# Kernel tuning notes

Measured on AMD Instinct MI355X. Metric: run time of the kernel, lower is better.

The kernel has to match this reference:

```python
import jax, jax.numpy as jnp
import numpy as np

EMBED_DIM = 64
NUM_ITEM = 1000000
BATCH = 131072
SEQ_LEN = 5
# fixed_arc = "AND,0,~1;OR,2,3;AND,5,6;OR,~7,4" parsed: (module, (pos, negated), (pos, negated))
ARC = [("AND", (0, False), (1, True)),
       ("OR",  (2, False), (3, False)),
       ("AND", (5, False), (6, False)),
       ("OR",  (7, True),  (4, False))]


def setup_inputs() -> dict:
    key = jax.random.key(0)
    ks = jax.random.split(key, 20)
    std = 0.01  # init_params: normal(0, 0.01)
    inp = {}
    inp["seq"] = jax.random.randint(ks[0], (BATCH, SEQ_LEN), 0, NUM_ITEM, dtype=jnp.int32)
    inp["pos_target"] = jax.random.randint(ks[1], (BATCH,), 0, NUM_ITEM, dtype=jnp.int32)
    inp["neg_target"] = jax.random.randint(ks[2], (BATCH,), 0, NUM_ITEM, dtype=jnp.int32)
    inp["item_embed"] = std * jax.random.normal(ks[3], (NUM_ITEM, EMBED_DIM), dtype=jnp.float32)
    t = jax.random.uniform(ks[4], (EMBED_DIM,), minval=0.0, maxval=0.1, dtype=jnp.float32)
    inp["true_vec"] = t / jnp.maximum(jnp.linalg.norm(t), 1e-12)
    inp["not_W1"] = std * jax.random.normal(ks[5], (EMBED_DIM, EMBED_DIM), dtype=jnp.float32)
    inp["not_b1"] = std * jax.random.normal(ks[6], (EMBED_DIM,), dtype=jnp.float32)
    inp["not_W2"] = std * jax.random.normal(ks[7], (EMBED_DIM, EMBED_DIM), dtype=jnp.float32)
    inp["not_b2"] = std * jax.random.normal(ks[8], (EMBED_DIM,), dtype=jnp.float32)
    inp["and_W1"] = std * jax.random.normal(ks[9], (2 * EMBED_DIM, EMBED_DIM), dtype=jnp.float32)
    inp["and_b1"] = std * jax.random.normal(ks[10], (EMBED_DIM,), dtype=jnp.float32)
    inp["and_W2"] = std * jax.random.normal(ks[11], (EMBED_DIM, EMBED_DIM), dtype=jnp.float32)
    inp["and_b2"] = std * jax.random.normal(ks[12], (EMBED_DIM,), dtype=jnp.float32)
    inp["or_W1"] = std * jax.random.normal(ks[13], (2 * EMBED_DIM, EMBED_DIM), dtype=jnp.float32)
    inp["or_b1"] = std * jax.random.normal(ks[14], (EMBED_DIM,), dtype=jnp.float32)
    inp["or_W2"] = std * jax.random.normal(ks[15], (EMBED_DIM, EMBED_DIM), dtype=jnp.float32)
    inp["or_b2"] = std * jax.random.normal(ks[16], (EMBED_DIM,), dtype=jnp.float32)
    return inp


def _mlp(x, W1, b1, W2, b2):
    # _get_ln_module(num_layers=2, dropout=0): Linear -> LeakyReLU -> Dropout(0) -> Linear
    h = jax.nn.leaky_relu(x @ W1 + b1, negative_slope=0.01)
    return h @ W2 + b2


def reference(seq, pos_target, neg_target, item_embed, true_vec,
              not_W1, not_b1, not_W2, not_b2,
              and_W1, and_b1, and_W2, and_b2,
              or_W1, or_b1, or_W2, or_b2):
    NOT = lambda x: _mlp(x, not_W1, not_b1, not_W2, not_b2)
    AND = lambda x: _mlp(x, and_W1, and_b1, and_W2, and_b2)
    OR = lambda x: _mlp(x, or_W1, or_b1, or_W2, or_b2)
    mods = {"AND": AND, "OR": OR}

    intermediates = {}

    def get_input(pos, neg):
        if pos < SEQ_LEN:
            e = item_embed[seq[:, pos]]  # [B, D] embedding gather
        else:
            e = intermediates[pos]
        return NOT(e) if neg else e

    out = None
    for layer_id, (name, (p1, n1), (p2, n2)) in enumerate(ARC):
        i1 = get_input(p1, n1)
        i2 = get_input(p2, n2)
        out = mods[name](jnp.concatenate((i1, i2), axis=-1))
        intermediates[SEQ_LEN + layer_id] = out

    enc_not = NOT(out)  # [B, D]
    pos_e = item_embed[pos_target]
    neg_e = item_embed[neg_target]
    encoded_pos = OR(jnp.concatenate((enc_not, pos_e), axis=-1))
    encoded_neg = OR(jnp.concatenate((enc_not, neg_e), axis=-1))
    encoded = jnp.concatenate((encoded_pos, encoded_neg), axis=0)  # [2B, D]

    # cosine similarity vs 'true' anchor, amplified by 10 (cos_amplify_factor)
    eps = 1e-8
    num = encoded @ true_vec
    denom = jnp.maximum(jnp.linalg.norm(encoded, axis=-1), eps) * jnp.maximum(jnp.linalg.norm(true_vec), eps)
    prediction = (num / denom) * 10.0
    return prediction
```

## Files before the change

### kernel.cpp

```cpp
#include <hip/hip_runtime.h>
#include <stdint.h>
#include <math.h>

#define BATCH 131072

typedef __attribute__((ext_vector_type(8)))  short short8;
typedef __attribute__((ext_vector_type(16))) float float16;

#define WS_LO_OFF 65536
#define WS_TN_OFF 131072

__global__ __launch_bounds__(256)
void prep_kernel(const float* __restrict__ tvec,
                 const float* __restrict__ nW1, const float* __restrict__ nW2,
                 const float* __restrict__ aW1, const float* __restrict__ aW2,
                 const float* __restrict__ oW1, const float* __restrict__ oW2,
                 char* __restrict__ ws)
{
    const int id = blockIdx.x * 256 + threadIdx.x;
    if (id == 0) {
        float s = 0.f;
        for (int j = 0; j < 64; ++j) s = fmaf(tvec[j], tvec[j], s);
        *(float*)(ws + WS_TN_OFF) = fmaxf(sqrtf(s), 1e-8f);
    }
    const float* srcs[8] = { nW1, nW2, aW1, aW1 + 4096, aW2, oW1, oW1 + 4096, oW2 };
    const int u    = id >> 12;
    const int e    = id & 4095;
    const int j    = e & 7;
    const int lane = (e >> 3) & 63;
    const int f    = e >> 9;
    const int nt   = f & 1, kc = f >> 1;
    const int k    = kc * 16 + (lane >> 5) * 8 + j;
    const int n    = nt * 32 + (lane & 31);
    const float v  = srcs[u][k * 64 + n];
    const uint32_t b  = __float_as_uint(v);
    const uint32_t hb = b & 0xffff0000u;
    const uint32_t lo = __float_as_uint(v - __uint_as_float(hb));
    ((uint16_t*)(ws + u * 8192 + f * 1024 + lane * 16))[j]             = (uint16_t)(b  >> 16);
    ((uint16_t*)(ws + WS_LO_OFF + u * 8192 + f * 1024 + lane * 16))[j] = (uint16_t)(lo >> 16);
}

union S8 { short8 s; uint32_t u[4]; };
union F8 { float f[8]; uint32_t u[8]; float4 v4[2]; };

struct Frag { short8 hi[4]; short8 lo[4]; };

__global__ __launch_bounds__(256)
void logicnet_mfma(const int* __restrict__ seq, const int* __restrict__ post,
                   const int* __restrict__ negt, const float* __restrict__ E,
                   const float* __restrict__ tvec,
                   const float* __restrict__ nb1, const float* __restrict__ nb2,
                   const float* __restrict__ ab1, const float* __restrict__ ab2,
                   const float* __restrict__ ob1, const float* __restrict__ ob2,
                   const char* __restrict__ ws, float* __restrict__ out)
{
    __shared__ uint32_t lds[4 * 2112];
    const int tid  = threadIdx.x;
    const int wid  = tid >> 6;
    const int lane = tid & 63;
    const int m    = lane & 31;
    const int h    = lane >> 5;
    const int tile = blockIdx.x * 4 + wid;
    const int rowbase = tile * 32;
    uint32_t* const stage = &lds[wid * 2112];

    const float tn = *(const float*)(ws + WS_TN_OFF);

    float nb1v[2] = { nb1[m], nb1[32 + m] };
    float nb2v[2] = { nb2[m], nb2[32 + m] };
    float ab1v[2] = { ab1[m], ab1[32 + m] };
    float ab2v[2] = { ab2[m], ab2[32 + m] };
    float ob1v[2] = { ob1[m], ob1[32 + m] };
    float ob2v[2] = { ob2[m], ob2[32 + m] };

    const int rr = rowbase + m;
    const int s0 = seq[rr * 5 + 0], s1i = seq[rr * 5 + 1], s2 = seq[rr * 5 + 2];
    const int s3 = seq[rr * 5 + 3], s4 = seq[rr * 5 + 4];
    const int ip = post[rr], im = negt[rr];

    float16 acc[2], accE[2];

    auto initacc = [&](const float* bv) {
#pragma unroll
        for (int nt = 0; nt < 2; ++nt)
#pragma unroll
            for (int i = 0; i < 16; ++i) acc[nt][i] = bv[nt];
    };

    auto ua = [&](const Frag& x, int u) {
        const char* base = ws + u * 8192 + lane * 16;
#pragma unroll
        for (int kc = 0; kc < 4; ++kc) {
#pragma unroll
            for (int nt = 0; nt < 2; ++nt) {
                const int off = (kc * 2 + nt) * 1024;
                short8 whi = *(const short8*)(base + off);
                short8 wlo = *(const short8*)(base + WS_LO_OFF + off);
                acc[nt] = __builtin_amdgcn_mfma_f32_32x32x16_bf16(x.hi[kc], whi, acc[nt], 0, 0, 0);
                acc[nt] = __builtin_amdgcn_mfma_f32_32x32x16_bf16(x.lo[kc], whi, acc[nt], 0, 0, 0);
                acc[nt] = __builtin_amdgcn_mfma_f32_32x32x16_bf16(x.hi[kc], wlo, acc[nt], 0, 0, 0);
            }
        }
    };

    auto epi_store = [&](bool lrelu) {
#pragma unroll
        for (int nt = 0; nt < 2; ++nt) {
            const int c = nt * 32 + m;
#pragma unroll
            for (int g = 0; g < 4; ++g)
#pragma unroll
                for (int q = 0; q < 4; ++q) {
                    const int r = q + 8 * g + 4 * h;
                    float v = acc[nt][g * 4 + q];
                    if (lrelu) v = fmaxf(v, 0.01f * v);
                    const uint32_t uu = __float_as_uint(v);
                    const uint32_t hb = uu & 0xffff0000u;
                    const uint32_t lo = __float_as_uint(v - __uint_as_float(hb));
                    stage[r * 66 + c] = hb | (lo >> 16);
                }
        }
    };

    auto load_frags = [&](Frag& x) {
#pragma unroll
        for (int kc = 0; kc < 4; ++kc) {
            const uint32_t* p = &stage[m * 66 + kc * 16 + h * 8];
            uint32_t w[8];
#pragma unroll
            for (int i = 0; i < 8; ++i) w[i] = p[i];
            S8 hi, lo;
#pragma unroll
            for (int i = 0; i < 4; ++i) {
                hi.u[i] = (w[2 * i] >> 16)      | (w[2 * i + 1] & 0xffff0000u);
                lo.u[i] = (w[2 * i] & 0xffffu)  | (w[2 * i + 1] << 16);
            }
            x.hi[kc] = hi.s; x.lo[kc] = lo.s;
        }
    };

    auto gather = [&](int idx, Frag& x) {
        const float4* e = (const float4*)(E + (size_t)idx * 64 + h * 8);
#pragma unroll
        for (int kc = 0; kc < 4; ++kc) {
            F8 xf8;
            xf8.v4[0] = e[kc * 4];
            xf8.v4[1] = e[kc * 4 + 1];
            uint32_t lu[8];
#pragma unroll
            for (int i = 0; i < 8; ++i) {
                const float hf = __uint_as_float(xf8.u[i] & 0xffff0000u);
                lu[i] = __float_as_uint(xf8.f[i] - hf);
            }
            S8 hi, lo;
#pragma unroll
            for (int i = 0; i < 4; ++i) {
                hi.u[i] = (xf8.u[2 * i] >> 16) | (xf8.u[2 * i + 1] & 0xffff0000u);
                lo.u[i] = (lu[2 * i] >> 16)    | (lu[2 * i + 1] & 0xffff0000u);
            }
            x.hi[kc] = hi.s; x.lo[kc] = lo.s;
        }
    };

    auto epi_reduce = [&](float* outp) {
#pragma unroll
        for (int nt = 0; nt < 2; ++nt) {
            const int c = nt * 32 + m;
#pragma unroll
            for (int g = 0; g < 4; ++g)
#pragma unroll
                for (int q = 0; q < 4; ++q) {
                    const int r = q + 8 * g + 4 * h;
                    stage[r * 66 + c] = __float_as_uint(acc[nt][g * 4 + q]);
                }
        }
        float num = 0.f, ss = 0.f;
        const float* tp = tvec + h * 32;
        const uint32_t* xp = &stage[m * 66 + h * 32];
#pragma unroll
        for (int i = 0; i < 32; i += 2) {
            const float x0 = __uint_as_float(xp[i]);
            const float x1 = __uint_as_float(xp[i + 1]);
            num = fmaf(x0, tp[i], fmaf(x1, tp[i + 1], num));
            ss  = fmaf(x0, x0, fmaf(x1, x1, ss));
        }
        num += __shfl_xor(num, 32, 64);
        ss  += __shfl_xor(ss, 32, 64);
        if (h == 0) outp[m] = num / (fmaxf(sqrtf(ss), 1e-8f) * tn) * 10.0f;
    };

    Frag xf, i6f;

    gather(s2, xf); initacc(ob1v); ua(xf, 5);
    gather(s3, xf); ua(xf, 6);
    epi_store(true);  load_frags(xf);
    initacc(ob2v); ua(xf, 7);
    epi_store(false); load_frags(i6f);

    gather(s1i, xf); initacc(nb1v); ua(xf, 0);
    epi_store(true);  load_frags(xf);
    initacc(nb2v); ua(xf, 1);
    epi_store(false); load_frags(xf);

    initacc(ab1v); ua(xf, 3);
    gather(s0, xf); ua(xf, 2);
    epi_store(true);  load_frags(xf);
    initacc(ab2v); ua(xf, 4);
    epi_store(false); load_frags(xf);

    initacc(ab1v); ua(xf, 2); ua(i6f, 3);
    epi_store(true);  load_frags(xf);
    initacc(ab2v); ua(xf, 4);
    epi_store(false); load_frags(xf);

    initacc(nb1v); ua(xf, 0);
    epi_store(true);  load_frags(xf);
    initacc(nb2v); ua(xf, 1);
    epi_store(false); load_frags(xf);

    initacc(ob1v); ua(xf, 5);
    gather(s4, xf); ua(xf, 6);
    epi_store(true);  load_frags(xf);
    initacc(ob2v); ua(xf, 7);
    epi_store(false); load_frags(xf);

    initacc(nb1v); ua(xf, 0);
    epi_store(true);  load_frags(xf);
    initacc(nb2v); ua(xf, 1);
    epi_store(false); load_frags(xf);

    initacc(ob1v); ua(xf, 5);
    accE[0] = acc[0]; accE[1] = acc[1];

    gather(ip, xf); ua(xf, 6);
    epi_store(true);  load_frags(xf);
    initacc(ob2v); ua(xf, 7);
    epi_reduce(out + rowbase);

    acc[0] = accE[0]; acc[1] = accE[1];
    gather(im, xf); ua(xf, 6);
    epi_store(true);  load_frags(xf);
    initacc(ob2v); ua(xf, 7);
    epi_reduce(out + BATCH + rowbase);
}

extern "C" void kernel_launch(void* const* d_in, const int* in_sizes, int n_in,
                              void* d_out, int out_size, void* d_ws, size_t ws_size,
                              hipStream_t stream) {
    const int*   seq  = (const int*)  d_in[0];
    const int*   post = (const int*)  d_in[1];
    const int*   negt = (const int*)  d_in[2];
    const float* E    = (const float*)d_in[3];
    const float* tv   = (const float*)d_in[4];
    const float* nW1  = (const float*)d_in[5];
    const float* nb1  = (const float*)d_in[6];
    const float* nW2  = (const float*)d_in[7];
    const float* nb2  = (const float*)d_in[8];
    const float* aW1  = (const float*)d_in[9];
    const float* ab1  = (const float*)d_in[10];
    const float* aW2  = (const float*)d_in[11];
    const float* ab2  = (const float*)d_in[12];
    const float* oW1  = (const float*)d_in[13];
    const float* ob1  = (const float*)d_in[14];
    const float* oW2  = (const float*)d_in[15];
    const float* ob2  = (const float*)d_in[16];
    float* out = (float*)d_out;
    char*  ws  = (char*)d_ws;

    hipLaunchKernelGGL(prep_kernel, dim3(128), dim3(256), 0, stream,
                       tv, nW1, nW2, aW1, aW2, oW1, oW2, ws);
    hipLaunchKernelGGL(logicnet_mfma, dim3(BATCH / 128), dim3(256), 0, stream,
                       seq, post, negt, E, tv,
                       nb1, nb2, ab1, ab2, ob1, ob2, ws, out);
}
```

Measured before the change: 486.3 us.

## Drive MLP chain from an op table to cut register pressure

Replaces the fully unrolled sequence of gathers and MLP stages with a non-unrolled loop over a packed 23-entry op table. Gathered embeddings are written straight to LDS in packed hi/lo form, and fragments are built from LDS inside each matmul instead of being kept in registers. Biases are staged into the workspace by the prep kernel, and launch bounds request 4 blocks per CU. The goal is to shrink code size and VGPR use to raise occupancy and hide gather latency. The cost is runtime branching, extra LDS traffic, and less freedom for the compiler to schedule across stages.

```diff
diff --git a/kernel.cpp b/kernel.cpp
--- a/kernel.cpp
+++ b/kernel.cpp
@@ -3,18 +3,24 @@
 #include <math.h>
 
 #define BATCH 131072
+#define WS_LO_OFF 65536
+#define WS_TN_OFF 131072
+#define WS_B_OFF  131080
 
 typedef __attribute__((ext_vector_type(8)))  short short8;
 typedef __attribute__((ext_vector_type(16))) float float16;
 
-#define WS_LO_OFF 65536
-#define WS_TN_OFF 131072
+union S8 { short8 s; uint32_t u[4]; };
+union F8 { float f[8]; uint32_t u[8]; float4 v4[2]; };
 
 __global__ __launch_bounds__(256)
 void prep_kernel(const float* __restrict__ tvec,
                  const float* __restrict__ nW1, const float* __restrict__ nW2,
                  const float* __restrict__ aW1, const float* __restrict__ aW2,
                  const float* __restrict__ oW1, const float* __restrict__ oW2,
+                 const float* __restrict__ nb1, const float* __restrict__ nb2,
+                 const float* __restrict__ ab1, const float* __restrict__ ab2,
+                 const float* __restrict__ ob1, const float* __restrict__ ob2,
                  char* __restrict__ ws)
 {
     const int id = blockIdx.x * 256 + threadIdx.x;
@@ -23,87 +29,110 @@
         for (int j = 0; j < 64; ++j) s = fmaf(tvec[j], tvec[j], s);
         *(float*)(ws + WS_TN_OFF) = fmaxf(sqrtf(s), 1e-8f);
     }
-    const float* srcs[8] = { nW1, nW2, aW1, aW1 + 4096, aW2, oW1, oW1 + 4096, oW2 };
-    const int u    = id >> 12;
-    const int e    = id & 4095;
-    const int j    = e & 7;
-    const int lane = (e >> 3) & 63;
-    const int f    = e >> 9;
-    const int nt   = f & 1, kc = f >> 1;
-    const int k    = kc * 16 + (lane >> 5) * 8 + j;
-    const int n    = nt * 32 + (lane & 31);
-    const float v  = srcs[u][k * 64 + n];
-    const uint32_t b  = __float_as_uint(v);
-    const uint32_t hb = b & 0xffff0000u;
-    const uint32_t lo = __float_as_uint(v - __uint_as_float(hb));
-    ((uint16_t*)(ws + u * 8192 + f * 1024 + lane * 16))[j]             = (uint16_t)(b  >> 16);
-    ((uint16_t*)(ws + WS_LO_OFF + u * 8192 + f * 1024 + lane * 16))[j] = (uint16_t)(lo >> 16);
+    if (id < 32768) {
+        const float* srcs[8] = { nW1, nW2, aW1, aW1 + 4096, aW2, oW1, oW1 + 4096, oW2 };
+        const int u    = id >> 12;
+        const int e    = id & 4095;
+        const int j    = e & 7;
+        const int lane = (e >> 3) & 63;
+        const int f    = e >> 9;
+        const int nt   = f & 1, kc = f >> 1;
+        const int k    = kc * 16 + (lane >> 5) * 8 + j;
+        const int n    = nt * 32 + (lane & 31);
+        const float v  = srcs[u][k * 64 + n];
+        const uint32_t b  = __float_as_uint(v);
+        const uint32_t hb = b & 0xffff0000u;
+        const uint32_t lo = __float_as_uint(v - __uint_as_float(hb));
+        ((uint16_t*)(ws + u * 8192 + f * 1024 + lane * 16))[j]             = (uint16_t)(b  >> 16);
+        ((uint16_t*)(ws + WS_LO_OFF + u * 8192 + f * 1024 + lane * 16))[j] = (uint16_t)(lo >> 16);
+    } else if (id < 33152) {
+        const int b   = id - 32768;
+        const int arr = b >> 6, j = b & 63;
+        const float* bp = (arr == 0) ? nb1 : (arr == 1) ? nb2 : (arr == 2) ? ab1
+                        : (arr == 3) ? ab2 : (arr == 4) ? ob1 : ob2;
+        ((float*)(ws + WS_B_OFF))[b] = bp[j];
+    }
 }
 
-union S8 { short8 s; uint32_t u[4]; };
-union F8 { float f[8]; uint32_t u[8]; float4 v4[2]; };
-
-struct Frag { short8 hi[4]; short8 lo[4]; };
-
-__global__ __launch_bounds__(256)
+#define OP(u,g,ik,tb,ek,bd) ((u)|((g)<<3)|((ik)<<6)|((tb)<<8)|((ek)<<9)|((bd)<<12))
+
+__global__ __launch_bounds__(256, 4)
 void logicnet_mfma(const int* __restrict__ seq, const int* __restrict__ post,
                    const int* __restrict__ negt, const float* __restrict__ E,
                    const float* __restrict__ tvec,
-                   const float* __restrict__ nb1, const float* __restrict__ nb2,
-                   const float* __restrict__ ab1, const float* __restrict__ ab2,
-                   const float* __restrict__ ob1, const float* __restrict__ ob2,
                    const char* __restrict__ ws, float* __restrict__ out)
 {
+    static const uint32_t PROG[23] = {
+        OP(0,2,1,0,1,0),
+        OP(1,0,1,0,2,1),
+        OP(3,0,1,0,0,2),
+        OP(2,1,0,0,1,0),
+        OP(4,0,1,0,2,3),
+        OP(2,0,3,1,0,2),
+        OP(5,3,1,0,0,4),
+        OP(6,4,0,0,1,0),
+        OP(7,0,1,0,2,5),
+        OP(3,0,0,1,1,0),
+        OP(4,0,1,0,2,3),
+        OP(0,0,1,0,1,0),
+        OP(1,0,1,0,2,1),
+        OP(5,0,1,0,0,4),
+        OP(6,5,0,0,1,0),
+        OP(7,0,1,0,2,5),
+        OP(0,0,1,0,1,0),
+        OP(1,0,1,0,2,1),
+        OP(5,0,3,1,0,4),
+        OP(6,6,2,0,1,0),
+        OP(7,0,1,0,4,5),
+        OP(6,7,2,0,1,0),
+        OP(7,0,1,0,5,5),
+    };
+
     __shared__ uint32_t lds[4 * 2112];
     const int tid  = threadIdx.x;
     const int wid  = tid >> 6;
     const int lane = tid & 63;
     const int m    = lane & 31;
     const int h    = lane >> 5;
-    const int tile = blockIdx.x * 4 + wid;
-    const int rowbase = tile * 32;
+    const int rowbase = (blockIdx.x * 4 + wid) * 32;
+    const int rr   = rowbase + m;
     uint32_t* const stage = &lds[wid * 2112];
 
-    const float tn = *(const float*)(ws + WS_TN_OFF);
-
-    float nb1v[2] = { nb1[m], nb1[32 + m] };
-    float nb2v[2] = { nb2[m], nb2[32 + m] };
-    float ab1v[2] = { ab1[m], ab1[32 + m] };
-    float ab2v[2] = { ab2[m], ab2[32 + m] };
-    float ob1v[2] = { ob1[m], ob1[32 + m] };
-    float ob2v[2] = { ob2[m], ob2[32 + m] };
-
-    const int rr = rowbase + m;
-    const int s0 = seq[rr * 5 + 0], s1i = seq[rr * 5 + 1], s2 = seq[rr * 5 + 2];
-    const int s3 = seq[rr * 5 + 3], s4 = seq[rr * 5 + 4];
-    const int ip = post[rr], im = negt[rr];
-
-    float16 acc[2], accE[2];
-
-    auto initacc = [&](const float* bv) {
-#pragma unroll
-        for (int nt = 0; nt < 2; ++nt)
-#pragma unroll
-            for (int i = 0; i < 16; ++i) acc[nt][i] = bv[nt];
-    };
-
-    auto ua = [&](const Frag& x, int u) {
-        const char* base = ws + u * 8192 + lane * 16;
+    const float  tn  = *(const float*)(ws + WS_TN_OFF);
+    const float* wsb = (const float*)(ws + WS_B_OFF);
+
+    float16 acc[2], accB[2];
+
+    auto ua = [&](float16* A, int u) {
+        const char* wb = ws + u * 8192 + lane * 16;
 #pragma unroll
         for (int kc = 0; kc < 4; ++kc) {
+            const uint2* p2 = (const uint2*)&stage[m * 66 + kc * 16 + h * 8];
+            uint2 a0 = p2[0], a1 = p2[1], a2 = p2[2], a3 = p2[3];
+            const uint32_t w0 = a0.x, w1 = a0.y, w2 = a1.x, w3 = a1.y;
+            const uint32_t w4 = a2.x, w5 = a2.y, w6 = a3.x, w7 = a3.y;
+            S8 xhi, xlo;
+            xhi.u[0] = (w0 >> 16) | (w1 & 0xffff0000u);
+            xhi.u[1] = (w2 >> 16) | (w3 & 0xffff0000u);
+            xhi.u[2] = (w4 >> 16) | (w5 & 0xffff0000u);
+            xhi.u[3] = (w6 >> 16) | (w7 & 0xffff0000u);
+            xlo.u[0] = (w0 & 0xffffu) | (w1 << 16);
+            xlo.u[1] = (w2 & 0xffffu) | (w3 << 16);
+            xlo.u[2] = (w4 & 0xffffu) | (w5 << 16);
+            xlo.u[3] = (w6 & 0xffffu) | (w7 << 16);
 #pragma unroll
             for (int nt = 0; nt < 2; ++nt) {
                 const int off = (kc * 2 + nt) * 1024;
-                short8 whi = *(const short8*)(base + off);
-                short8 wlo = *(const short8*)(base + WS_LO_OFF + off);
-                acc[nt] = __builtin_amdgcn_mfma_f32_32x32x16_bf16(x.hi[kc], whi, acc[nt], 0, 0, 0);
-                acc[nt] = __builtin_amdgcn_mfma_f32_32x32x16_bf16(x.lo[kc], whi, acc[nt], 0, 0, 0);
-                acc[nt] = __builtin_amdgcn_mfma_f32_32x32x16_bf16(x.hi[kc], wlo, acc[nt], 0, 0, 0);
+                short8 whi = *(const short8*)(wb + off);
+                short8 wlo = *(const short8*)(wb + WS_LO_OFF + off);
+                A[nt] = __builtin_amdgcn_mfma_f32_32x32x16_bf16(xhi.s, whi, A[nt], 0, 0, 0);
+                A[nt] = __builtin_amdgcn_mfma_f32_32x32x16_bf16(xlo.s, whi, A[nt], 0, 0, 0);
+                A[nt] = __builtin_amdgcn_mfma_f32_32x32x16_bf16(xhi.s, wlo, A[nt], 0, 0, 0);
             }
         }
     };
 
-    auto epi_store = [&](bool lrelu) {
+    auto epi_store = [&](const float16* A, bool act) {
 #pragma unroll
         for (int nt = 0; nt < 2; ++nt) {
             const int c = nt * 32 + m;
@@ -112,8 +141,8 @@
 #pragma unroll
                 for (int q = 0; q < 4; ++q) {
                     const int r = q + 8 * g + 4 * h;
-                    float v = acc[nt][g * 4 + q];
-                    if (lrelu) v = fmaxf(v, 0.01f * v);
+                    float v = A[nt][g * 4 + q];
+                    if (act) v = fmaxf(v, 0.01f * v);
                     const uint32_t uu = __float_as_uint(v);
                     const uint32_t hb = uu & 0xffff0000u;
                     const uint32_t lo = __float_as_uint(v - __uint_as_float(hb));
@@ -122,43 +151,30 @@
         }
     };
 
-    auto load_frags = [&](Frag& x) {
-#pragma unroll
-        for (int kc = 0; kc < 4; ++kc) {
-            const uint32_t* p = &stage[m * 66 + kc * 16 + h * 8];
-            uint32_t w[8];
-#pragma unroll
-            for (int i = 0; i < 8; ++i) w[i] = p[i];
-            S8 hi, lo;
-#pragma unroll
-            for (int i = 0; i < 4; ++i) {
-                hi.u[i] = (w[2 * i] >> 16)      | (w[2 * i + 1] & 0xffff0000u);
-                lo.u[i] = (w[2 * i] & 0xffffu)  | (w[2 * i + 1] << 16);
-            }
-            x.hi[kc] = hi.s; x.lo[kc] = lo.s;
-        }
-    };
-
-    auto gather = [&](int idx, Frag& x) {
+    auto gwrite = [&](int g) {
+        int idx;
+        if (g < 6)      idx = seq[(size_t)rr * 5 + (g - 1)];
+        else if (g == 6) idx = post[rr];
+        else             idx = negt[rr];
         const float4* e = (const float4*)(E + (size_t)idx * 64 + h * 8);
 #pragma unroll
         for (int kc = 0; kc < 4; ++kc) {
             F8 xf8;
             xf8.v4[0] = e[kc * 4];
             xf8.v4[1] = e[kc * 4 + 1];
-            uint32_t lu[8];
+            uint32_t pk[8];
 #pragma unroll
             for (int i = 0; i < 8; ++i) {
-                const float hf = __uint_as_float(xf8.u[i] & 0xffff0000u);
-                lu[i] = __float_as_uint(xf8.f[i] - hf);
+                const uint32_t b  = xf8.u[i];
+                const uint32_t hb = b & 0xffff0000u;
+                const uint32_t lo = __float_as_uint(xf8.f[i] - __uint_as_float(hb));
+                pk[i] = hb | (lo >> 16);
             }
-            S8 hi, lo;
-#pragma unroll
-            for (int i = 0; i < 4; ++i) {
-                hi.u[i] = (xf8.u[2 * i] >> 16) | (xf8.u[2 * i + 1] & 0xffff0000u);
-                lo.u[i] = (lu[2 * i] >> 16)    | (lu[2 * i + 1] & 0xffff0000u);
-            }
-            x.hi[kc] = hi.s; x.lo[kc] = lo.s;
+            uint2* q = (uint2*)&stage[m * 66 + kc * 16 + h * 8];
+            q[0] = make_uint2(pk[0], pk[1]);
+            q[1] = make_uint2(pk[2], pk[3]);
+            q[2] = make_uint2(pk[4], pk[5]);
+            q[3] = make_uint2(pk[6], pk[7]);
         }
     };
 
@@ -189,59 +205,38 @@
         if (h == 0) outp[m] = num / (fmaxf(sqrtf(ss), 1e-8f) * tn) * 10.0f;
     };
 
-    Frag xf, i6f;
-
-    gather(s2, xf); initacc(ob1v); ua(xf, 5);
-    gather(s3, xf); ua(xf, 6);
-    epi_store(true);  load_frags(xf);
-    initacc(ob2v); ua(xf, 7);
-    epi_store(false); load_frags(i6f);
-
-    gather(s1i, xf); initacc(nb1v); ua(xf, 0);
-    epi_store(true);  load_frags(xf);
-    initacc(nb2v); ua(xf, 1);
-    epi_store(false); load_frags(xf);
-
-    initacc(ab1v); ua(xf, 3);
-    gather(s0, xf); ua(xf, 2);
-    epi_store(true);  load_frags(xf);
-    initacc(ab2v); ua(xf, 4);
-    epi_store(false); load_frags(xf);
-
-    initacc(ab1v); ua(xf, 2); ua(i6f, 3);
-    epi_store(true);  load_frags(xf);
-    initacc(ab2v); ua(xf, 4);
-    epi_store(false); load_frags(xf);
-
-    initacc(nb1v); ua(xf, 0);
-    epi_store(true);  load_frags(xf);
-    initacc(nb2v); ua(xf, 1);
-    epi_store(false); load_frags(xf);
-
-    initacc(ob1v); ua(xf, 5);
-    gather(s4, xf); ua(xf, 6);
-    epi_store(true);  load_frags(xf);
-    initacc(ob2v); ua(xf, 7);
-    epi_store(false); load_frags(xf);
-
-    initacc(nb1v); ua(xf, 0);
-    epi_store(true);  load_frags(xf);
-    initacc(nb2v); ua(xf, 1);
-    epi_store(false); load_frags(xf);
-
-    initacc(ob1v); ua(xf, 5);
-    accE[0] = acc[0]; accE[1] = acc[1];
-
-    gather(ip, xf); ua(xf, 6);
-    epi_store(true);  load_frags(xf);
-    initacc(ob2v); ua(xf, 7);
-    epi_reduce(out + rowbase);
-
-    acc[0] = accE[0]; acc[1] = accE[1];
-    gather(im, xf); ua(xf, 6);
-    epi_store(true);  load_frags(xf);
-    initacc(ob2v); ua(xf, 7);
-    epi_reduce(out + BATCH + rowbase);
+#pragma unroll 1
+    for (int op = 0; op < 23; ++op) {
+        const uint32_t cw  = PROG[op];
+        const int u     = cw & 7;
+        const int g     = (cw >> 3) & 7;
+        const int initk = (cw >> 6) & 3;
+        const int toB   = (cw >> 8) & 1;
+        const int epik  = (cw >> 9) & 7;
+        const int bid   = (cw >> 12) & 7;
+
+        if (g) gwrite(g);
+
+        if (initk == 1) {
+            const float b0 = wsb[bid * 64 + m], b1 = wsb[bid * 64 + 32 + m];
+#pragma unroll
+            for (int i = 0; i < 16; ++i) { acc[0][i] = b0; acc[1][i] = b1; }
+        } else if (initk == 2) {
+#pragma unroll
+            for (int i = 0; i < 16; ++i) { acc[0][i] = accB[0][i]; acc[1][i] = accB[1][i]; }
+        } else if (initk == 3) {
+            const float b0 = wsb[bid * 64 + m], b1 = wsb[bid * 64 + 32 + m];
+#pragma unroll
+            for (int i = 0; i < 16; ++i) { accB[0][i] = b0; accB[1][i] = b1; }
+        }
+
+        if (toB) ua(accB, u); else ua(acc, u);
+
+        if (epik == 1)      epi_store(toB ? accB : acc, true);
+        else if (epik == 2) epi_store(toB ? accB : acc, false);
+        else if (epik == 4) epi_reduce(out + rowbase);
+        else if (epik == 5) epi_reduce(out + BATCH + rowbase);
+    }
 }
 
 extern "C" void kernel_launch(void* const* d_in, const int* in_sizes, int n_in,
@@ -267,9 +262,9 @@
     float* out = (float*)d_out;
     char*  ws  = (char*)d_ws;
 
-    hipLaunchKernelGGL(prep_kernel, dim3(128), dim3(256), 0, stream,
-                       tv, nW1, nW2, aW1, aW2, oW1, oW2, ws);
+    hipLaunchKernelGGL(prep_kernel, dim3(130), dim3(256), 0, stream,
+                       tv, nW1, nW2, aW1, aW2, oW1, oW2,
+                       nb1, nb2, ab1, ab2, ob1, ob2, ws);
     hipLaunchKernelGGL(logicnet_mfma, dim3(BATCH / 128), dim3(256), 0, stream,
-                       seq, post, negt, E, tv,
-                       nb1, nb2, ab1, ab2, ob1, ob2, ws, out);
+                       seq, post, negt, E, tv, ws, out);
 }
```

Result: slower. 1.143 ms (+135.1%).
